# Performance work log

Measured on AMD Instinct MI355X. Metric: run time of the kernel, lower is better.

Reference implementation:

```python
import jax, jax.numpy as jnp
import numpy as np

G = 8
SCALE = 0.125
RESID = 1.0
EPS = 1e-5


def setup_inputs() -> dict:
    key = jax.random.key(0)
    ks = jax.random.split(key, 9)
    B, C, D = 64, 512, 1024
    s = 0.02
    return {
        "inp_q": jax.random.normal(ks[0], (B, C, D), jnp.float32),
        "inp_k": jax.random.normal(ks[1], (B, C, D), jnp.float32),
        "inp_v": jax.random.normal(ks[2], (B, C, D), jnp.float32),
        "Wt": jax.random.normal(ks[3], (C, C), jnp.float32) * s,
        "Wp": jax.random.normal(ks[4], (C, C), jnp.float32) * s,
        "Wg": jax.random.normal(ks[5], (C, C), jnp.float32) * s,
        "Wz": jax.random.normal(ks[6], (G, C // G, C // G), jnp.float32) * s,
        "gamma": jax.random.normal(ks[7], (C,), jnp.float32),
        "beta": jax.random.normal(ks[8], (C,), jnp.float32),
    }


def reference(inp_q, inp_k, inp_v, Wt, Wp, Wg, Wz, gamma, beta):
    b, C, d = inp_v.shape
    cg = C // G
    # 1x1 conv1d projections == per-position GEMM over channels
    t = jnp.einsum('oc,bcd->bod', Wt, inp_v)  # (b, C, d)
    p = jnp.einsum('oc,bcd->bod', Wp, inp_q)
    g = jnp.einsum('oc,bcd->bod', Wg, inp_k)
    tg = t.reshape(b, G, cg, d)
    pg = p.reshape(b, G, cg, d)
    gg = g.reshape(b, G, cg, d)
    # CGNL dot-product kernel: rank-1 reduction to scalar per (batch, group)
    att = jnp.einsum('bgcd,bgcd->bg', pg, gg) * SCALE  # (b, G)
    x = att[:, :, None, None] * tg  # (b, G, cg, d)
    # grouped 1x1 conv z (groups=G)
    x = jnp.einsum('goc,bgcd->bgod', Wz, x)  # (b, G, cg, d)
    # GroupNorm(num_groups=G) over (cg, d) per group
    mean = x.mean(axis=(2, 3), keepdims=True)
    var = x.var(axis=(2, 3), keepdims=True)
    xn = (x - mean) / jnp.sqrt(var + EPS)
    xn = xn.reshape(b, C, d) * gamma[None, :, None] + beta[None, :, None]
    return xn + inp_v * RESID
```

## Files before the change

kernel.cpp:

```cpp
#include <hip/hip_runtime.h>
#include <hip/hip_bf16.h>

#define G_ 8
#define SCALE_ 0.125f
#define EPS_ 1e-5f
#define BATCH 64
#define CCH 512
#define DD 1024

typedef __attribute__((ext_vector_type(8))) short short8;
typedef __attribute__((ext_vector_type(4))) short short4v;
typedef __attribute__((ext_vector_type(4))) float float4v;

__device__ __forceinline__ unsigned short bf16_rne(float f) {
    union { float f; unsigned u; } x; x.f = f;
    unsigned u = x.u;
    unsigned r = (u + 0x7fffu + ((u >> 16) & 1u)) >> 16;
    return (unsigned short)r;
}
__device__ __forceinline__ float bf16_to_f(unsigned short h) {
    union { unsigned u; float f; } x; x.u = ((unsigned)h) << 16;
    return x.f;
}

__global__ void zero_att_kernel(float* att) {
    int t = threadIdx.x;
    if (t < 512) {
        att[t]         = 0.0f;
        att[t + 512]   = 0.0f;
        att[t + 1024]  = 0.0f;
    }
}

__global__ __launch_bounds__(256) void w2_kernel(const float* __restrict__ Wt,
                                                 const float* __restrict__ Wz,
                                                 unsigned short* __restrict__ W2bf) {
    int idx = blockIdx.x * 256 + threadIdx.x;
    int c  = idx & 511;
    int og = idx >> 9;
    int g  = og >> 6;
    int o  = og & 63;
    const float* wz = Wz + (g * 64 + o) * 64;
    const float* wt = Wt + (size_t)(g * 64) * 512 + c;
    float acc = 0.0f;
#pragma unroll 8
    for (int cg = 0; cg < 64; ++cg) acc += wz[cg] * wt[(size_t)cg * 512];
    W2bf[idx] = bf16_rne(acc);
}

__global__ __launch_bounds__(256) void m2_kernel(const float* __restrict__ Wp,
                                                 const float* __restrict__ Wg,
                                                 float* __restrict__ M2) {
    __shared__ __align__(16) float Ap[64][64];
    __shared__ __align__(16) float Bg[64][64];
    int g  = blockIdx.x & 7;
    int tj = (blockIdx.x >> 3) & 7;
    int ti = blockIdx.x >> 6;
    int i0 = ti * 64, j0 = tj * 64;
    int tid = threadIdx.x;
    int tx = tid & 15, ty = tid >> 4;
#pragma unroll
    for (int r = 0; r < 16; ++r) {
        int f = tid + r * 256;
        int o = f >> 6, col = f & 63;
        Ap[o][col] = Wp[(size_t)(g * 64 + o) * 512 + i0 + col];
        Bg[o][col] = Wg[(size_t)(g * 64 + o) * 512 + j0 + col];
    }
    __syncthreads();
    float acc[4][4] = {};
#pragma unroll 4
    for (int o = 0; o < 64; ++o) {
        float4v av = *(const float4v*)&Ap[o][ty * 4];
        float4v bv = *(const float4v*)&Bg[o][tx * 4];
#pragma unroll
        for (int a = 0; a < 4; ++a)
#pragma unroll
            for (int b = 0; b < 4; ++b) acc[a][b] += av[a] * bv[b];
    }
#pragma unroll
    for (int a = 0; a < 4; ++a)
#pragma unroll
        for (int b = 0; b < 4; ++b)
            M2[((size_t)(i0 + ty * 4 + a) * 512 + (j0 + tx * 4 + b)) * 8 + g] = acc[a][b];
}

#define LDK 40

__global__ __launch_bounds__(256) void sgemm_att_kernel(const float* __restrict__ q,
                                                        const float* __restrict__ kmat,
                                                        const float* __restrict__ M2,
                                                        float* __restrict__ att) {
    __shared__ __align__(16) short Ah[128 * LDK];
    __shared__ __align__(16) short Al[128 * LDK];
    __shared__ __align__(16) short Bh[128 * LDK];
    __shared__ __align__(16) short Bl[128 * LDK];
    __shared__ float red[256 * 8];

    int b  = blockIdx.y;
    int i0 = (blockIdx.x & 3) * 128;
    int j0 = (blockIdx.x >> 2) * 128;
    const float* qb = q    + (size_t)b * CCH * DD;
    const float* kb = kmat + (size_t)b * CCH * DD;

    int tid  = threadIdx.x;
    int wave = tid >> 6, lane = tid & 63;
    int quad = lane >> 4, l15 = lane & 15;
    int wm = (wave >> 1) * 64, wn = (wave & 1) * 64;

    float4v acc[4][4];
#pragma unroll
    for (int a = 0; a < 4; ++a)
#pragma unroll
        for (int c = 0; c < 4; ++c) acc[a][c] = (float4v){0.f, 0.f, 0.f, 0.f};

    for (int kt = 0; kt < DD; kt += 32) {
#pragma unroll
        for (int r = 0; r < 4; ++r) {
            int f   = tid + r * 256;
            int row = f >> 3;
            int c4  = (f & 7) * 4;
            float4v qa = *(const float4v*)(qb + (size_t)(i0 + row) * DD + kt + c4);
            float4v ka = *(const float4v*)(kb + (size_t)(j0 + row) * DD + kt + c4);
            short4v qh, ql, kh, kl;
#pragma unroll
            for (int e = 0; e < 4; ++e) {
                float x = qa[e];
                unsigned short h = bf16_rne(x);
                qh[e] = (short)h;
                ql[e] = (short)bf16_rne(x - bf16_to_f(h));
                float y = ka[e];
                unsigned short h2 = bf16_rne(y);
                kh[e] = (short)h2;
                kl[e] = (short)bf16_rne(y - bf16_to_f(h2));
            }
            *(short4v*)&Ah[row * LDK + c4] = qh;
            *(short4v*)&Al[row * LDK + c4] = ql;
            *(short4v*)&Bh[row * LDK + c4] = kh;
            *(short4v*)&Bl[row * LDK + c4] = kl;
        }
        __syncthreads();

        short8 ah[4], al[4], bh8[4], bl8[4];
#pragma unroll
        for (int mi = 0; mi < 4; ++mi) {
            int rr = wm + mi * 16 + l15;
            ah[mi] = *(const short8*)&Ah[rr * LDK + quad * 8];
            al[mi] = *(const short8*)&Al[rr * LDK + quad * 8];
        }
#pragma unroll
        for (int ni = 0; ni < 4; ++ni) {
            int rr = wn + ni * 16 + l15;
            bh8[ni] = *(const short8*)&Bh[rr * LDK + quad * 8];
            bl8[ni] = *(const short8*)&Bl[rr * LDK + quad * 8];
        }
#pragma unroll
        for (int mi = 0; mi < 4; ++mi)
#pragma unroll
            for (int ni = 0; ni < 4; ++ni) {
                acc[mi][ni] = __builtin_amdgcn_mfma_f32_16x16x32_bf16(ah[mi], bh8[ni], acc[mi][ni], 0, 0, 0);
                acc[mi][ni] = __builtin_amdgcn_mfma_f32_16x16x32_bf16(al[mi], bh8[ni], acc[mi][ni], 0, 0, 0);
                acc[mi][ni] = __builtin_amdgcn_mfma_f32_16x16x32_bf16(ah[mi], bl8[ni], acc[mi][ni], 0, 0, 0);
            }
        __syncthreads();
    }

    float r8[8] = {};
#pragma unroll
    for (int mi = 0; mi < 4; ++mi)
#pragma unroll
        for (int ni = 0; ni < 4; ++ni)
#pragma unroll
            for (int r = 0; r < 4; ++r) {
                int i = i0 + wm + mi * 16 + quad * 4 + r;
                int j = j0 + wn + ni * 16 + l15;
                float s = acc[mi][ni][r];
                const float* mp = M2 + ((size_t)i * 512 + j) * 8;
                float4v m0 = *(const float4v*)mp;
                float4v m1 = *(const float4v*)(mp + 4);
                r8[0] += s * m0[0]; r8[1] += s * m0[1]; r8[2] += s * m0[2]; r8[3] += s * m0[3];
                r8[4] += s * m1[0]; r8[5] += s * m1[1]; r8[6] += s * m1[2]; r8[7] += s * m1[3];
            }
#pragma unroll
    for (int g8 = 0; g8 < 8; ++g8) red[tid * 8 + g8] = r8[g8];
    __syncthreads();
    for (int off = 128; off > 0; off >>= 1) {
        if (tid < off) {
#pragma unroll
            for (int g8 = 0; g8 < 8; ++g8) red[tid * 8 + g8] += red[(tid + off) * 8 + g8];
        }
        __syncthreads();
    }
    if (tid < 8) atomicAdd(&att[b * 8 + tid], red[tid]);
}

__global__ __launch_bounds__(512, 4) void ygemm_kernel(const unsigned short* __restrict__ W2bf,
                                                       const float* __restrict__ v,
                                                       float* __restrict__ y,
                                                       float* __restrict__ ysum,
                                                       float* __restrict__ ysum2) {
    __shared__ __align__(16) short As[256 * LDK];
    __shared__ __align__(16) short Bs[128 * LDK];

    int b  = blockIdx.y;
    int o0 = (blockIdx.x & 1) * 256;
    int d0 = (blockIdx.x >> 1) * 128;
    const float* vb = v + (size_t)b * CCH * DD;

    int tid  = threadIdx.x;
    int wave = tid >> 6, lane = tid & 63;
    int quad = lane >> 4, l15 = lane & 15;
    int wo = wave >> 1, wd = wave & 1;

    float4v acc[4][4];
#pragma unroll
    for (int a = 0; a < 4; ++a)
#pragma unroll
        for (int c = 0; c < 4; ++c) acc[a][c] = (float4v){0.f, 0.f, 0.f, 0.f};

    int nB = tid & 127;
    int kB = (tid >> 7) * 8;

    for (int kt = 0; kt < CCH; kt += 32) {
#pragma unroll
        for (int r = 0; r < 2; ++r) {
            int f   = tid + r * 512;
            int row = f >> 2;
            int c8  = (f & 3) * 8;
            short8 w = *(const short8*)(W2bf + (size_t)(o0 + row) * 512 + kt + c8);
            *(short8*)&As[row * LDK + c8] = w;
        }
        {
            short8 bsv;
#pragma unroll
            for (int jj = 0; jj < 8; ++jj) {
                float f = vb[(size_t)(kt + kB + jj) * DD + d0 + nB];
                bsv[jj] = (short)bf16_rne(f);
            }
            *(short8*)&Bs[nB * LDK + kB] = bsv;
        }
        __syncthreads();

        short8 af[4], bf[4];
#pragma unroll
        for (int mi = 0; mi < 4; ++mi)
            af[mi] = *(const short8*)&As[(wo * 64 + mi * 16 + l15) * LDK + quad * 8];
#pragma unroll
        for (int ni = 0; ni < 4; ++ni)
            bf[ni] = *(const short8*)&Bs[(wd * 64 + ni * 16 + l15) * LDK + quad * 8];
#pragma unroll
        for (int mi = 0; mi < 4; ++mi)
#pragma unroll
            for (int ni = 0; ni < 4; ++ni)
                acc[mi][ni] = __builtin_amdgcn_mfma_f32_16x16x32_bf16(af[mi], bf[ni], acc[mi][ni], 0, 0, 0);
        __syncthreads();
    }

    float* yb = y + (size_t)b * CCH * DD;
    float s = 0.f, s2 = 0.f;
#pragma unroll
    for (int mi = 0; mi < 4; ++mi)
#pragma unroll
        for (int ni = 0; ni < 4; ++ni) {
            int o = o0 + wo * 64 + mi * 16 + quad * 4;
            int d = d0 + wd * 64 + ni * 16 + l15;
#pragma unroll
            for (int r = 0; r < 4; ++r) {
                float val = acc[mi][ni][r];
                yb[(size_t)(o + r) * DD + d] = val;
                s  += val;
                s2 += val * val;
            }
        }
#pragma unroll
    for (int off = 32; off > 0; off >>= 1) {
        s  += __shfl_down(s, off, 64);
        s2 += __shfl_down(s2, off, 64);
    }
    if (lane == 0) {
        int g = (o0 >> 6) + wo;
        atomicAdd(&ysum[b * 8 + g], s);
        atomicAdd(&ysum2[b * 8 + g], s2);
    }
}

__global__ void finalize_kernel(const float* __restrict__ att,
                                const float* __restrict__ ysum,
                                const float* __restrict__ ysum2,
                                float* __restrict__ scl,
                                float* __restrict__ meanp) {
    int bg = threadIdx.x;
    if (bg < 512) {
        float inv = 1.0f / 65536.0f;
        float m = ysum[bg] * inv;
        float var = ysum2[bg] * inv - m * m;
        float a = att[bg] * SCALE_;
        scl[bg] = a / sqrtf(a * a * var + EPS_);
        meanp[bg] = m;
    }
}

__global__ __launch_bounds__(256) void final_kernel(const float* __restrict__ v,
                                                    const float* __restrict__ gamma,
                                                    const float* __restrict__ beta,
                                                    const float* __restrict__ scl,
                                                    const float* __restrict__ meanp,
                                                    float* __restrict__ out) {
    size_t idx = ((size_t)blockIdx.x * 256 + threadIdx.x) * 4;
    int c  = (int)((idx >> 10) & 511);
    int bg = (int)(idx >> 19) * 8 + (c >> 6);
    float4v y4 = *(const float4v*)(out + idx);
    float4v v4 = *(const float4v*)(v + idx);
    float sc = scl[bg] * gamma[c];
    float sh = beta[c] - sc * meanp[bg];
    float4v o4;
    o4[0] = y4[0] * sc + sh + v4[0];
    o4[1] = y4[1] * sc + sh + v4[1];
    o4[2] = y4[2] * sc + sh + v4[2];
    o4[3] = y4[3] * sc + sh + v4[3];
    *(float4v*)(out + idx) = o4;
}

extern "C" void kernel_launch(void* const* d_in, const int* in_sizes, int n_in,
                              void* d_out, int out_size, void* d_ws, size_t ws_size,
                              hipStream_t stream) {
    const float* q     = (const float*)d_in[0];
    const float* kmat  = (const float*)d_in[1];
    const float* v     = (const float*)d_in[2];
    const float* Wt    = (const float*)d_in[3];
    const float* Wp    = (const float*)d_in[4];
    const float* Wg    = (const float*)d_in[5];
    const float* Wz    = (const float*)d_in[6];
    const float* gamma = (const float*)d_in[7];
    const float* beta  = (const float*)d_in[8];
    float* out = (float*)d_out;

    char* ws = (char*)d_ws;
    float*          M2    = (float*)ws;
    unsigned short* W2bf  = (unsigned short*)(ws + 8388608);
    float*          att   = (float*)(ws + 8912896);
    float*          ysum  = (float*)(ws + 8914944);
    float*          ysum2 = (float*)(ws + 8916992);
    float*          scl   = (float*)(ws + 8919040);
    float*          meanp = (float*)(ws + 8921088);

    hipLaunchKernelGGL(zero_att_kernel, dim3(1), dim3(512), 0, stream, att);
    hipLaunchKernelGGL(w2_kernel, dim3(1024), dim3(256), 0, stream, Wt, Wz, W2bf);
    hipLaunchKernelGGL(m2_kernel, dim3(512), dim3(256), 0, stream, Wp, Wg, M2);
    hipLaunchKernelGGL(sgemm_att_kernel, dim3(16, 64), dim3(256), 0, stream, q, kmat, M2, att);
    hipLaunchKernelGGL(ygemm_kernel, dim3(16, 64), dim3(512), 0, stream, W2bf, v, out, ysum, ysum2);
    hipLaunchKernelGGL(finalize_kernel, dim3(1), dim3(512), 0, stream, att, ysum, ysum2, scl, meanp);
    hipLaunchKernelGGL(final_kernel, dim3(32768), dim3(256), 0, stream, v, gamma, beta, scl, meanp, out);
}
```

Baseline: 732.2 us.

## Swizzle LDS tiles, remap blocks for XCD locality, truncate split-bf16, shuffle reductions

Replaces the padded LDS layout (stride 40) with an XOR-swizzled 32-wide layout in both GEMM kernels, which shrinks shared memory and aims to avoid bank conflicts. Blocks are launched on a 1D grid and remapped so consecutive batches land on the same XCD, for L2 locality. The hi/lo bf16 split of q/k now uses truncation instead of RNE, which cuts ALU work while keeping the residual exact enough. It also adds a launch-bounds occupancy hint, reorders the MFMA loop to lower register pressure, and replaces the shared-memory tree reduction with wave shuffles. Truncation slightly changes the numerics of the split.

```diff
diff --git a/kernel.cpp b/kernel.cpp
--- a/kernel.cpp
+++ b/kernel.cpp
@@ -18,17 +18,19 @@
     unsigned r = (u + 0x7fffu + ((u >> 16) & 1u)) >> 16;
     return (unsigned short)r;
 }
-__device__ __forceinline__ float bf16_to_f(unsigned short h) {
-    union { unsigned u; float f; } x; x.u = ((unsigned)h) << 16;
-    return x.f;
-}
+__device__ __forceinline__ short f2bf(float f) {
+    __hip_bfloat16 h = __float2bfloat16(f);
+    return *reinterpret_cast<short*>(&h);
+}
+
+#define SWZI(row, so) ((((row) * 32) + (so)) ^ (((row) & 14) << 2))
 
 __global__ void zero_att_kernel(float* att) {
     int t = threadIdx.x;
     if (t < 512) {
-        att[t]         = 0.0f;
-        att[t + 512]   = 0.0f;
-        att[t + 1024]  = 0.0f;
+        att[t]        = 0.0f;
+        att[t + 512]  = 0.0f;
+        att[t + 1024] = 0.0f;
     }
 }
 
@@ -45,7 +47,7 @@
     float acc = 0.0f;
 #pragma unroll 8
     for (int cg = 0; cg < 64; ++cg) acc += wz[cg] * wt[(size_t)cg * 512];
-    W2bf[idx] = bf16_rne(acc);
+    W2bf[idx] = (unsigned short)f2bf(acc);
 }
 
 __global__ __launch_bounds__(256) void m2_kernel(const float* __restrict__ Wp,
@@ -84,21 +86,22 @@
             M2[((size_t)(i0 + ty * 4 + a) * 512 + (j0 + tx * 4 + b)) * 8 + g] = acc[a][b];
 }
 
-#define LDK 40
-
-__global__ __launch_bounds__(256) void sgemm_att_kernel(const float* __restrict__ q,
-                                                        const float* __restrict__ kmat,
-                                                        const float* __restrict__ M2,
-                                                        float* __restrict__ att) {
-    __shared__ __align__(16) short Ah[128 * LDK];
-    __shared__ __align__(16) short Al[128 * LDK];
-    __shared__ __align__(16) short Bh[128 * LDK];
-    __shared__ __align__(16) short Bl[128 * LDK];
-    __shared__ float red[256 * 8];
-
-    int b  = blockIdx.y;
-    int i0 = (blockIdx.x & 3) * 128;
-    int j0 = (blockIdx.x >> 2) * 128;
+__global__ __launch_bounds__(256, 4) void sgemm_att_kernel(const float* __restrict__ q,
+                                                           const float* __restrict__ kmat,
+                                                           const float* __restrict__ M2,
+                                                           float* __restrict__ att) {
+    __shared__ __align__(16) short Ah[128 * 32];
+    __shared__ __align__(16) short Al[128 * 32];
+    __shared__ __align__(16) short Bh[128 * 32];
+    __shared__ __align__(16) short Bl[128 * 32];
+    __shared__ float wred[4][8];
+
+    int bid = blockIdx.x;
+    int swz = (bid & 7) * 128 + (bid >> 3);
+    int b  = swz >> 4;
+    int t  = swz & 15;
+    int i0 = (t & 3) * 128;
+    int j0 = (t >> 2) * 128;
     const float* qb = q    + (size_t)b * CCH * DD;
     const float* kb = kmat + (size_t)b * CCH * DD;
 
@@ -107,6 +110,11 @@
     int quad = lane >> 4, l15 = lane & 15;
     int wm = (wave >> 1) * 64, wn = (wave & 1) * 64;
 
+    int srow = tid >> 3;
+    int sc4  = (tid & 7) * 4;
+    const float* qp0 = qb + (size_t)(i0 + srow) * DD + sc4;
+    const float* kp0 = kb + (size_t)(j0 + srow) * DD + sc4;
+
     float4v acc[4][4];
 #pragma unroll
     for (int a = 0; a < 4; ++a)
@@ -116,51 +124,50 @@
     for (int kt = 0; kt < DD; kt += 32) {
 #pragma unroll
         for (int r = 0; r < 4; ++r) {
-            int f   = tid + r * 256;
-            int row = f >> 3;
-            int c4  = (f & 7) * 4;
-            float4v qa = *(const float4v*)(qb + (size_t)(i0 + row) * DD + kt + c4);
-            float4v ka = *(const float4v*)(kb + (size_t)(j0 + row) * DD + kt + c4);
+            int row = srow + r * 32;
+            float4v qa = *(const float4v*)(qp0 + (size_t)r * 32 * DD + kt);
+            float4v ka = *(const float4v*)(kp0 + (size_t)r * 32 * DD + kt);
             short4v qh, ql, kh, kl;
 #pragma unroll
             for (int e = 0; e < 4; ++e) {
-                float x = qa[e];
-                unsigned short h = bf16_rne(x);
-                qh[e] = (short)h;
-                ql[e] = (short)bf16_rne(x - bf16_to_f(h));
-                float y = ka[e];
-                unsigned short h2 = bf16_rne(y);
-                kh[e] = (short)h2;
-                kl[e] = (short)bf16_rne(y - bf16_to_f(h2));
-            }
-            *(short4v*)&Ah[row * LDK + c4] = qh;
-            *(short4v*)&Al[row * LDK + c4] = ql;
-            *(short4v*)&Bh[row * LDK + c4] = kh;
-            *(short4v*)&Bl[row * LDK + c4] = kl;
+                union { float f; unsigned u; } cq; cq.f = qa[e];
+                union { float f; unsigned u; } ck; ck.f = ka[e];
+                qh[e] = (short)(cq.u >> 16);
+                kh[e] = (short)(ck.u >> 16);
+                union { unsigned u; float f; } hq; hq.u = cq.u & 0xffff0000u;
+                union { unsigned u; float f; } hk; hk.u = ck.u & 0xffff0000u;
+                union { float f; unsigned u; } rq; rq.f = qa[e] - hq.f;
+                union { float f; unsigned u; } rk; rk.f = ka[e] - hk.f;
+                ql[e] = (short)(rq.u >> 16);
+                kl[e] = (short)(rk.u >> 16);
+            }
+            int wi = SWZI(row, sc4);
+            *(short4v*)&Ah[wi] = qh;
+            *(short4v*)&Al[wi] = ql;
+            *(short4v*)&Bh[wi] = kh;
+            *(short4v*)&Bl[wi] = kl;
         }
         __syncthreads();
 
-        short8 ah[4], al[4], bh8[4], bl8[4];
+        short8 ah[4], al[4];
 #pragma unroll
         for (int mi = 0; mi < 4; ++mi) {
-            int rr = wm + mi * 16 + l15;
-            ah[mi] = *(const short8*)&Ah[rr * LDK + quad * 8];
-            al[mi] = *(const short8*)&Al[rr * LDK + quad * 8];
+            int ri = SWZI(wm + mi * 16 + l15, quad * 8);
+            ah[mi] = *(const short8*)&Ah[ri];
+            al[mi] = *(const short8*)&Al[ri];
         }
 #pragma unroll
         for (int ni = 0; ni < 4; ++ni) {
-            int rr = wn + ni * 16 + l15;
-            bh8[ni] = *(const short8*)&Bh[rr * LDK + quad * 8];
-            bl8[ni] = *(const short8*)&Bl[rr * LDK + quad * 8];
-        }
-#pragma unroll
-        for (int mi = 0; mi < 4; ++mi)
-#pragma unroll
-            for (int ni = 0; ni < 4; ++ni) {
-                acc[mi][ni] = __builtin_amdgcn_mfma_f32_16x16x32_bf16(ah[mi], bh8[ni], acc[mi][ni], 0, 0, 0);
-                acc[mi][ni] = __builtin_amdgcn_mfma_f32_16x16x32_bf16(al[mi], bh8[ni], acc[mi][ni], 0, 0, 0);
-                acc[mi][ni] = __builtin_amdgcn_mfma_f32_16x16x32_bf16(ah[mi], bl8[ni], acc[mi][ni], 0, 0, 0);
-            }
+            int ri = SWZI(wn + ni * 16 + l15, quad * 8);
+            short8 bh8 = *(const short8*)&Bh[ri];
+            short8 bl8 = *(const short8*)&Bl[ri];
+#pragma unroll
+            for (int mi = 0; mi < 4; ++mi) {
+                acc[mi][ni] = __builtin_amdgcn_mfma_f32_16x16x32_bf16(ah[mi], bh8, acc[mi][ni], 0, 0, 0);
+                acc[mi][ni] = __builtin_amdgcn_mfma_f32_16x16x32_bf16(al[mi], bh8, acc[mi][ni], 0, 0, 0);
+                acc[mi][ni] = __builtin_amdgcn_mfma_f32_16x16x32_bf16(ah[mi], bl8, acc[mi][ni], 0, 0, 0);
+            }
+        }
         __syncthreads();
     }
 
@@ -181,16 +188,16 @@
                 r8[4] += s * m1[0]; r8[5] += s * m1[1]; r8[6] += s * m1[2]; r8[7] += s * m1[3];
             }
 #pragma unroll
-    for (int g8 = 0; g8 < 8; ++g8) red[tid * 8 + g8] = r8[g8];
+    for (int off = 32; off > 0; off >>= 1)
+#pragma unroll
+        for (int g8 = 0; g8 < 8; ++g8)
+            r8[g8] += __shfl_down(r8[g8], off, 64);
+    if (lane == 0)
+#pragma unroll
+        for (int g8 = 0; g8 < 8; ++g8) wred[wave][g8] = r8[g8];
     __syncthreads();
-    for (int off = 128; off > 0; off >>= 1) {
-        if (tid < off) {
-#pragma unroll
-            for (int g8 = 0; g8 < 8; ++g8) red[tid * 8 + g8] += red[(tid + off) * 8 + g8];
-        }
-        __syncthreads();
-    }
-    if (tid < 8) atomicAdd(&att[b * 8 + tid], red[tid]);
+    if (tid < 8)
+        atomicAdd(&att[b * 8 + tid], wred[0][tid] + wred[1][tid] + wred[2][tid] + wred[3][tid]);
 }
 
 __global__ __launch_bounds__(512, 4) void ygemm_kernel(const unsigned short* __restrict__ W2bf,
@@ -198,12 +205,15 @@
                                                        float* __restrict__ y,
                                                        float* __restrict__ ysum,
                                                        float* __restrict__ ysum2) {
-    __shared__ __align__(16) short As[256 * LDK];
-    __shared__ __align__(16) short Bs[128 * LDK];
-
-    int b  = blockIdx.y;
-    int o0 = (blockIdx.x & 1) * 256;
-    int d0 = (blockIdx.x >> 1) * 128;
+    __shared__ __align__(16) short As[256 * 32];
+    __shared__ __align__(16) short Bs[128 * 32];
+
+    int bid = blockIdx.x;
+    int swz = (bid & 7) * 128 + (bid >> 3);
+    int b  = swz >> 4;
+    int t  = swz & 15;
+    int o0 = (t & 1) * 256;
+    int d0 = (t >> 1) * 128;
     const float* vb = v + (size_t)b * CCH * DD;
 
     int tid  = threadIdx.x;
@@ -227,26 +237,26 @@
             int row = f >> 2;
             int c8  = (f & 3) * 8;
             short8 w = *(const short8*)(W2bf + (size_t)(o0 + row) * 512 + kt + c8);
-            *(short8*)&As[row * LDK + c8] = w;
+            *(short8*)&As[SWZI(row, c8)] = w;
         }
         {
             short8 bsv;
 #pragma unroll
             for (int jj = 0; jj < 8; ++jj) {
                 float f = vb[(size_t)(kt + kB + jj) * DD + d0 + nB];
-                bsv[jj] = (short)bf16_rne(f);
-            }
-            *(short8*)&Bs[nB * LDK + kB] = bsv;
+                bsv[jj] = f2bf(f);
+            }
+            *(short8*)&Bs[SWZI(nB, kB)] = bsv;
         }
         __syncthreads();
 
         short8 af[4], bf[4];
 #pragma unroll
         for (int mi = 0; mi < 4; ++mi)
-            af[mi] = *(const short8*)&As[(wo * 64 + mi * 16 + l15) * LDK + quad * 8];
+            af[mi] = *(const short8*)&As[SWZI(wo * 64 + mi * 16 + l15, quad * 8)];
 #pragma unroll
         for (int ni = 0; ni < 4; ++ni)
-            bf[ni] = *(const short8*)&Bs[(wd * 64 + ni * 16 + l15) * LDK + quad * 8];
+            bf[ni] = *(const short8*)&Bs[SWZI(wd * 64 + ni * 16 + l15, quad * 8)];
 #pragma unroll
         for (int mi = 0; mi < 4; ++mi)
 #pragma unroll
@@ -346,8 +356,8 @@
     hipLaunchKernelGGL(zero_att_kernel, dim3(1), dim3(512), 0, stream, att);
     hipLaunchKernelGGL(w2_kernel, dim3(1024), dim3(256), 0, stream, Wt, Wz, W2bf);
     hipLaunchKernelGGL(m2_kernel, dim3(512), dim3(256), 0, stream, Wp, Wg, M2);
-    hipLaunchKernelGGL(sgemm_att_kernel, dim3(16, 64), dim3(256), 0, stream, q, kmat, M2, att);
-    hipLaunchKernelGGL(ygemm_kernel, dim3(16, 64), dim3(512), 0, stream, W2bf, v, out, ysum, ysum2);
+    hipLaunchKernelGGL(sgemm_att_kernel, dim3(1024), dim3(256), 0, stream, q, kmat, M2, att);
+    hipLaunchKernelGGL(ygemm_kernel, dim3(1024), dim3(512), 0, stream, W2bf, v, out, ysum, ysum2);
     hipLaunchKernelGGL(finalize_kernel, dim3(1), dim3(512), 0, stream, att, ysum, ysum2, scl, meanp);
     hipLaunchKernelGGL(final_kernel, dim3(32768), dim3(256), 0, stream, v, gamma, beta, scl, meanp, out);
 }
```

Result: faster. 644.9 us (-11.9%).
